# Kernel optimization log

Hardware: AMD Instinct MI355X
Metric: run time of the kernel (lower is better)

The kernel has to match this reference:

```python
import jax, jax.numpy as jnp
import numpy as np

ALPHA = 1.0
LAMBDA_CL = 1.0
EPS = 1e-08


def setup_inputs() -> dict:
    key = jax.random.key(0)
    k1, k2, k3, k4 = jax.random.split(key, 4)
    N, D_IN, D_LAT, K = 16384, 1024, 128, 256
    x = jax.random.normal(k1, (N, D_IN), dtype=jnp.float32)
    h_x = jax.random.normal(k2, (N, D_LAT), dtype=jnp.float32)
    a_x = jax.random.normal(k3, (N, D_IN), dtype=jnp.float32)
    cluster_centers = jax.random.normal(k4, (K, D_LAT), dtype=jnp.float32)
    return {"x": x, "h_x": h_x, "a_x": a_x, "cluster_centers": cluster_centers}


def _pairwise_dist(h, R):
    # Euclidean cdist via ||h||^2 + ||R||^2 - 2 h R^T (avoids [N,K,d] broadcast)
    h2 = jnp.sum(h * h, axis=1, keepdims=True)            # [N,1]
    r2 = jnp.sum(R * R, axis=1)[None, :]                   # [1,K]
    d2 = h2 + r2 - 2.0 * jnp.einsum('nd,kd->nk', h, R)     # [N,K]
    return jnp.sqrt(jnp.maximum(d2, 0.0))


def reference(x, h_x, a_x, cluster_centers):
    # Reconstruction MSE
    loss_reconstr = jnp.mean((x - a_x) ** 2)
    # Alpha-smoothed soft assignments (note +EPS in denominator, as in original)
    dist = _pairwise_dist(h_x, cluster_centers)            # [N,K]
    e = jnp.exp(-ALPHA * dist)                             # [N,K]
    soft_assignments = e / (jnp.sum(e, axis=1, keepdims=True) + EPS)
    # Weighted centers and clustering MSE
    weighted_centers = jnp.einsum('nk,kd->nd', soft_assignments, cluster_centers)
    loss_clustering = jnp.mean((h_x - weighted_centers) ** 2)
    return loss_reconstr + LAMBDA_CL * loss_clustering
```

## Files before the change

kernel.cpp:

```cpp
#include <hip/hip_runtime.h>
#include <math.h>

#define N_ROWS 16384
#define D_INP  1024
#define D_LAT  128
#define KC     256
#define EPS_F  1e-8f

typedef __attribute__((ext_vector_type(8))) short short8v;
typedef _Float16 half8v __attribute__((ext_vector_type(8)));
typedef __attribute__((ext_vector_type(4))) float floatx4;
typedef __attribute__((ext_vector_type(4))) float f4v;

__device__ __forceinline__ unsigned short f2bf(float f) {
    unsigned u = __float_as_uint(f);
    return (unsigned short)((u + 0x7FFFu + ((u >> 16) & 1u)) >> 16);
}
__device__ __forceinline__ unsigned short f2h(float f) {
    _Float16 h = (_Float16)f;
    unsigned short u;
    __builtin_memcpy(&u, &h, 2);
    return u;
}

__global__ __launch_bounds__(256) void prep_kernel(const float* __restrict__ R,
        unsigned short* __restrict__ Rf16, unsigned short* __restrict__ Rtb,
        float* __restrict__ r2) {
    const int t = threadIdx.x;
    const int kc = blockIdx.x * 2 + (t >> 7);
    const int d = t & 127;
    const float v = R[kc * D_LAT + d];
    Rf16[kc * D_LAT + d] = f2h(v);
    Rtb[d * KC + kc] = f2bf(v);
    float sq = v * v;
    for (int off = 32; off > 0; off >>= 1) sq += __shfl_down(sq, off);
    __shared__ float s4[4];
    if ((t & 63) == 0) s4[t >> 6] = sq;
    __syncthreads();
    if (t == 0)   r2[kc] = s4[0] + s4[1];
    if (t == 128) r2[kc] = s4[2] + s4[3];
}

__global__ __launch_bounds__(512) void fused_kernel(
        const float* __restrict__ x, const float* __restrict__ a,
        const float* __restrict__ h,
        const unsigned short* __restrict__ Rf16,
        const unsigned short* __restrict__ Rtb,
        const float* __restrict__ r2w,
        float* __restrict__ pr, float* __restrict__ pc) {
    __shared__ float sh32[16 * 132];
    __shared__ unsigned short sh16[16 * 136];
    __shared__ unsigned short eL[16 * 264];
    __shared__ float sumsL[16][16];
    __shared__ float h2L[16];
    __shared__ float invL[16];
    __shared__ float swL[8];

    const int bid = blockIdx.x;
    const int tid = threadIdx.x;
    const int wv = tid >> 6, lane = tid & 63;

    if (bid & 1) {
        const int rid = bid >> 1;
        const int gid = rid * 512 + tid;
        const f4v* x4 = (const f4v*)x;
        const f4v* a4 = (const f4v*)a;
        float a0 = 0.f, a1 = 0.f, a2 = 0.f, a3 = 0.f;
#pragma unroll
        for (int it = 0; it < 8; ++it) {
            const int i = gid + it * (512 * 1024);
            const f4v xv = __builtin_nontemporal_load(x4 + i);
            const f4v av = __builtin_nontemporal_load(a4 + i);
            const float d0 = xv.x - av.x, d1 = xv.y - av.y;
            const float d2 = xv.z - av.z, d3 = xv.w - av.w;
            a0 = fmaf(d0, d0, a0);
            a1 = fmaf(d1, d1, a1);
            a2 = fmaf(d2, d2, a2);
            a3 = fmaf(d3, d3, a3);
        }
        float acc = (a0 + a1) + (a2 + a3);
        for (int off = 32; off > 0; off >>= 1) acc += __shfl_down(acc, off);
        if (lane == 0) swL[wv] = acc;
        __syncthreads();
        if (tid == 0) {
            float t = 0.f;
#pragma unroll
            for (int w = 0; w < 8; ++w) t += swL[w];
            pr[rid] = t;
        }
        return;
    }

    const int cid = bid >> 1;
    const int rbase = cid * 16;
    const int g = lane >> 4, c = lane & 15;

    {
        const int r = tid >> 5, c4 = tid & 31;
        const f4v v = __builtin_nontemporal_load(
            (const f4v*)(h + (size_t)(rbase + r) * D_LAT + c4 * 4));
        *(f4v*)&sh32[r * 132 + c4 * 4] = v;
        sh16[r * 136 + c4 * 4 + 0] = f2h(v.x);
        sh16[r * 136 + c4 * 4 + 1] = f2h(v.y);
        sh16[r * 136 + c4 * 4 + 2] = f2h(v.z);
        sh16[r * 136 + c4 * 4 + 3] = f2h(v.w);
        float s = v.x * v.x + v.y * v.y + v.z * v.z + v.w * v.w;
        s += __shfl_xor(s, 1);
        s += __shfl_xor(s, 2);
        s += __shfl_xor(s, 4);
        s += __shfl_xor(s, 8);
        s += __shfl_xor(s, 16);
        if ((tid & 31) == 0) h2L[r] = s;
    }
    __syncthreads();

    half8v afr[4];
#pragma unroll
    for (int ks = 0; ks < 4; ++ks)
        afr[ks] = *(const half8v*)&sh16[c * 136 + ks * 32 + g * 8];
    float h2a[4];
#pragma unroll
    for (int i = 0; i < 4; ++i) h2a[i] = h2L[4 * g + i];

#pragma unroll
    for (int tt = 0; tt < 2; ++tt) {
        const int tile = wv * 2 + tt;
        const int kc = tile * 16 + c;
        floatx4 acc = {0.f, 0.f, 0.f, 0.f};
#pragma unroll
        for (int ks = 0; ks < 4; ++ks) {
            const half8v b = *(const half8v*)(Rf16 + (size_t)kc * D_LAT + ks * 32 + g * 8);
            acc = __builtin_amdgcn_mfma_f32_16x16x32_f16(afr[ks], b, acc, 0, 0, 0);
        }
        const float r2v = r2w[kc];
#pragma unroll
        for (int i = 0; i < 4; ++i) {
            const float d2 = h2a[i] + r2v - 2.0f * acc[i];
            const float e = __expf(-sqrtf(fmaxf(d2, 0.f)));
            eL[(4 * g + i) * 264 + kc] = f2bf(e);
            float v = e;
            v += __shfl_xor(v, 1);
            v += __shfl_xor(v, 2);
            v += __shfl_xor(v, 4);
            v += __shfl_xor(v, 8);
            if (c == 0) sumsL[4 * g + i][tile] = v;
        }
    }
    __syncthreads();
    if (tid < 16) {
        float t = 0.f;
#pragma unroll
        for (int j = 0; j < 16; ++j) t += sumsL[tid][j];
        invL[tid] = 1.0f / (t + EPS_F);
    }
    __syncthreads();

    const int dcol = wv * 16 + c;
    float inva[4];
#pragma unroll
    for (int i = 0; i < 4; ++i) inva[i] = invL[4 * g + i];
    floatx4 acc = {0.f, 0.f, 0.f, 0.f};
#pragma unroll
    for (int ks = 0; ks < 8; ++ks) {
        const short8v ae = *(const short8v*)&eL[c * 264 + ks * 32 + g * 8];
        const short8v b = *(const short8v*)(Rtb + (size_t)dcol * KC + ks * 32 + g * 8);
        acc = __builtin_amdgcn_mfma_f32_16x16x32_bf16(ae, b, acc, 0, 0, 0);
    }
    float lp = 0.f;
#pragma unroll
    for (int i = 0; i < 4; ++i) {
        const float wc = acc[i] * inva[i];
        const float hv = sh32[(4 * g + i) * 132 + dcol];
        const float df = hv - wc;
        lp = fmaf(df, df, lp);
    }
    for (int off = 32; off > 0; off >>= 1) lp += __shfl_down(lp, off);
    if (lane == 0) swL[wv] = lp;
    __syncthreads();
    if (tid == 0) {
        float t = 0.f;
#pragma unroll
        for (int w = 0; w < 8; ++w) t += swL[w];
        pc[cid] = t;
    }
}

__global__ __launch_bounds__(256) void finalize_kernel(const float* __restrict__ pr,
                                                       const float* __restrict__ pc,
                                                       float* __restrict__ out) {
    const int tid = threadIdx.x;
    float a = 0.f, b = 0.f;
    for (int i = tid; i < 1024; i += 256) a += pr[i];
    for (int i = tid; i < 1024; i += 256) b += pc[i];
    float v = a * (1.0f / ((float)N_ROWS * (float)D_INP)) +
              b * (1.0f / ((float)N_ROWS * (float)D_LAT));
    for (int off = 32; off > 0; off >>= 1) v += __shfl_down(v, off);
    __shared__ float sw[4];
    if ((tid & 63) == 0) sw[tid >> 6] = v;
    __syncthreads();
    if (tid == 0) out[0] = sw[0] + sw[1] + sw[2] + sw[3];
}

extern "C" void kernel_launch(void* const* d_in, const int* in_sizes, int n_in,
                              void* d_out, int out_size, void* d_ws, size_t ws_size,
                              hipStream_t stream) {
    const float* x = (const float*)d_in[0];
    const float* h = (const float*)d_in[1];
    const float* a = (const float*)d_in[2];
    const float* R = (const float*)d_in[3];
    float* out = (float*)d_out;
    char* wsb = (char*)d_ws;
    float* pr = (float*)(wsb + 0);
    float* pc = (float*)(wsb + 8192);
    float* r2 = (float*)(wsb + 12288);
    unsigned short* Rf16 = (unsigned short*)(wsb + 16384);
    unsigned short* Rtb  = (unsigned short*)(wsb + 16384 + 65536);

    prep_kernel<<<128, 256, 0, stream>>>(R, Rf16, Rtb, r2);
    fused_kernel<<<2048, 512, 0, stream>>>(x, a, h, Rf16, Rtb, r2, pr, pc);
    finalize_kernel<<<1, 256, 0, stream>>>(pr, pc, out);
}
```

Baseline: 48.40 us.

## Process 64 rows per clustering block and rebalance block mix to 1:4

Each clustering block now handles 64 rows instead of 16. It loads the center fragments (Rf16 and a transposed fp16 copy) into registers once and reuses them across four row tiles, which cuts redundant global and L2 reads of the centers. The grid changes from alternating 1:1 to one clustering block per four reconstruction blocks (1280 total), and the reconstruction loads are batched before the arithmetic to raise memory-level parallelism. The second GEMM switches from bf16 to fp16, and the fp32 copy of h is dropped, so the residual now uses the fp16-rounded h. That costs some precision in exchange for less shared memory, which is now larger per block and may reduce occupancy.

```diff
diff --git a/kernel.cpp b/kernel.cpp
--- a/kernel.cpp
+++ b/kernel.cpp
@@ -7,31 +7,31 @@
 #define KC     256
 #define EPS_F  1e-8f
 
-typedef __attribute__((ext_vector_type(8))) short short8v;
 typedef _Float16 half8v __attribute__((ext_vector_type(8)));
 typedef __attribute__((ext_vector_type(4))) float floatx4;
 typedef __attribute__((ext_vector_type(4))) float f4v;
 
-__device__ __forceinline__ unsigned short f2bf(float f) {
-    unsigned u = __float_as_uint(f);
-    return (unsigned short)((u + 0x7FFFu + ((u >> 16) & 1u)) >> 16);
-}
 __device__ __forceinline__ unsigned short f2h(float f) {
     _Float16 h = (_Float16)f;
     unsigned short u;
     __builtin_memcpy(&u, &h, 2);
     return u;
 }
+__device__ __forceinline__ float h2f(unsigned short u) {
+    _Float16 h;
+    __builtin_memcpy(&h, &u, 2);
+    return (float)h;
+}
 
 __global__ __launch_bounds__(256) void prep_kernel(const float* __restrict__ R,
-        unsigned short* __restrict__ Rf16, unsigned short* __restrict__ Rtb,
+        unsigned short* __restrict__ Rf16, unsigned short* __restrict__ Rt16,
         float* __restrict__ r2) {
     const int t = threadIdx.x;
     const int kc = blockIdx.x * 2 + (t >> 7);
     const int d = t & 127;
     const float v = R[kc * D_LAT + d];
     Rf16[kc * D_LAT + d] = f2h(v);
-    Rtb[d * KC + kc] = f2bf(v);
+    Rt16[d * KC + kc] = f2h(v);
     float sq = v * v;
     for (int off = 32; off > 0; off >>= 1) sq += __shfl_down(sq, off);
     __shared__ float s4[4];
@@ -45,34 +45,37 @@
         const float* __restrict__ x, const float* __restrict__ a,
         const float* __restrict__ h,
         const unsigned short* __restrict__ Rf16,
-        const unsigned short* __restrict__ Rtb,
+        const unsigned short* __restrict__ Rt16,
         const float* __restrict__ r2w,
         float* __restrict__ pr, float* __restrict__ pc) {
-    __shared__ float sh32[16 * 132];
-    __shared__ unsigned short sh16[16 * 136];
-    __shared__ unsigned short eL[16 * 264];
-    __shared__ float sumsL[16][16];
-    __shared__ float h2L[16];
-    __shared__ float invL[16];
+    __shared__ unsigned short sh16[64 * 136];
+    __shared__ unsigned short eL[64 * 264];
+    __shared__ float sumsL[64][16];
+    __shared__ float h2L[64];
+    __shared__ float invL[64];
     __shared__ float swL[8];
 
     const int bid = blockIdx.x;
     const int tid = threadIdx.x;
     const int wv = tid >> 6, lane = tid & 63;
 
-    if (bid & 1) {
-        const int rid = bid >> 1;
+    if (bid % 5 != 0) {
+        const int rid = bid - 1 - bid / 5;
         const int gid = rid * 512 + tid;
         const f4v* x4 = (const f4v*)x;
         const f4v* a4 = (const f4v*)a;
-        float a0 = 0.f, a1 = 0.f, a2 = 0.f, a3 = 0.f;
+        f4v xv[8], av[8];
 #pragma unroll
         for (int it = 0; it < 8; ++it) {
             const int i = gid + it * (512 * 1024);
-            const f4v xv = __builtin_nontemporal_load(x4 + i);
-            const f4v av = __builtin_nontemporal_load(a4 + i);
-            const float d0 = xv.x - av.x, d1 = xv.y - av.y;
-            const float d2 = xv.z - av.z, d3 = xv.w - av.w;
+            xv[it] = __builtin_nontemporal_load(x4 + i);
+            av[it] = __builtin_nontemporal_load(a4 + i);
+        }
+        float a0 = 0.f, a1 = 0.f, a2 = 0.f, a3 = 0.f;
+#pragma unroll
+        for (int it = 0; it < 8; ++it) {
+            const float d0 = xv[it].x - av[it].x, d1 = xv[it].y - av[it].y;
+            const float d2 = xv[it].z - av[it].z, d3 = xv[it].w - av[it].w;
             a0 = fmaf(d0, d0, a0);
             a1 = fmaf(d1, d1, a1);
             a2 = fmaf(d2, d2, a2);
@@ -91,63 +94,77 @@
         return;
     }
 
-    const int cid = bid >> 1;
-    const int rbase = cid * 16;
+    const int cid = bid / 5;
+    const int rbase = cid * 64;
     const int g = lane >> 4, c = lane & 15;
 
     {
-        const int r = tid >> 5, c4 = tid & 31;
-        const f4v v = __builtin_nontemporal_load(
-            (const f4v*)(h + (size_t)(rbase + r) * D_LAT + c4 * 4));
-        *(f4v*)&sh32[r * 132 + c4 * 4] = v;
-        sh16[r * 136 + c4 * 4 + 0] = f2h(v.x);
-        sh16[r * 136 + c4 * 4 + 1] = f2h(v.y);
-        sh16[r * 136 + c4 * 4 + 2] = f2h(v.z);
-        sh16[r * 136 + c4 * 4 + 3] = f2h(v.w);
-        float s = v.x * v.x + v.y * v.y + v.z * v.z + v.w * v.w;
+        const int r = tid >> 3, c8 = tid & 7;
+        const float* hrow = h + (size_t)(rbase + r) * D_LAT;
+        float s = 0.f;
+#pragma unroll
+        for (int q = 0; q < 4; ++q) {
+            const int c4 = c8 + q * 8;
+            const f4v v = __builtin_nontemporal_load((const f4v*)(hrow + c4 * 4));
+            sh16[r * 136 + c4 * 4 + 0] = f2h(v.x);
+            sh16[r * 136 + c4 * 4 + 1] = f2h(v.y);
+            sh16[r * 136 + c4 * 4 + 2] = f2h(v.z);
+            sh16[r * 136 + c4 * 4 + 3] = f2h(v.w);
+            s = fmaf(v.x, v.x, s);
+            s = fmaf(v.y, v.y, s);
+            s = fmaf(v.z, v.z, s);
+            s = fmaf(v.w, v.w, s);
+        }
         s += __shfl_xor(s, 1);
         s += __shfl_xor(s, 2);
         s += __shfl_xor(s, 4);
-        s += __shfl_xor(s, 8);
-        s += __shfl_xor(s, 16);
-        if ((tid & 31) == 0) h2L[r] = s;
-    }
-    __syncthreads();
-
-    half8v afr[4];
-#pragma unroll
-    for (int ks = 0; ks < 4; ++ks)
-        afr[ks] = *(const half8v*)&sh16[c * 136 + ks * 32 + g * 8];
-    float h2a[4];
-#pragma unroll
-    for (int i = 0; i < 4; ++i) h2a[i] = h2L[4 * g + i];
-
-#pragma unroll
-    for (int tt = 0; tt < 2; ++tt) {
-        const int tile = wv * 2 + tt;
-        const int kc = tile * 16 + c;
-        floatx4 acc = {0.f, 0.f, 0.f, 0.f};
-#pragma unroll
-        for (int ks = 0; ks < 4; ++ks) {
-            const half8v b = *(const half8v*)(Rf16 + (size_t)kc * D_LAT + ks * 32 + g * 8);
-            acc = __builtin_amdgcn_mfma_f32_16x16x32_f16(afr[ks], b, acc, 0, 0, 0);
-        }
-        const float r2v = r2w[kc];
-#pragma unroll
-        for (int i = 0; i < 4; ++i) {
-            const float d2 = h2a[i] + r2v - 2.0f * acc[i];
-            const float e = __expf(-sqrtf(fmaxf(d2, 0.f)));
-            eL[(4 * g + i) * 264 + kc] = f2bf(e);
-            float v = e;
-            v += __shfl_xor(v, 1);
-            v += __shfl_xor(v, 2);
-            v += __shfl_xor(v, 4);
-            v += __shfl_xor(v, 8);
-            if (c == 0) sumsL[4 * g + i][tile] = v;
-        }
-    }
-    __syncthreads();
-    if (tid < 16) {
+        if ((tid & 7) == 0) h2L[r] = s;
+    }
+    __syncthreads();
+
+    {
+        half8v bA[2][4];
+#pragma unroll
+        for (int tt = 0; tt < 2; ++tt) {
+            const int kc = (wv * 2 + tt) * 16 + c;
+#pragma unroll
+            for (int ks = 0; ks < 4; ++ks)
+                bA[tt][ks] = *(const half8v*)(Rf16 + (size_t)kc * D_LAT + ks * 32 + g * 8);
+        }
+        const float r2v[2] = {r2w[wv * 32 + c], r2w[wv * 32 + 16 + c]};
+#pragma unroll
+        for (int rt = 0; rt < 4; ++rt) {
+            half8v aH[4];
+#pragma unroll
+            for (int ks = 0; ks < 4; ++ks)
+                aH[ks] = *(const half8v*)&sh16[(rt * 16 + c) * 136 + ks * 32 + g * 8];
+            float h2a[4];
+#pragma unroll
+            for (int i = 0; i < 4; ++i) h2a[i] = h2L[rt * 16 + 4 * g + i];
+#pragma unroll
+            for (int tt = 0; tt < 2; ++tt) {
+                floatx4 acc = {0.f, 0.f, 0.f, 0.f};
+#pragma unroll
+                for (int ks = 0; ks < 4; ++ks)
+                    acc = __builtin_amdgcn_mfma_f32_16x16x32_f16(aH[ks], bA[tt][ks], acc, 0, 0, 0);
+                const int kc = (wv * 2 + tt) * 16 + c;
+#pragma unroll
+                for (int i = 0; i < 4; ++i) {
+                    const float d2 = h2a[i] + r2v[tt] - 2.0f * acc[i];
+                    const float e = __expf(-sqrtf(fmaxf(d2, 0.f)));
+                    eL[(rt * 16 + 4 * g + i) * 264 + kc] = f2h(e);
+                    float v = e;
+                    v += __shfl_xor(v, 1);
+                    v += __shfl_xor(v, 2);
+                    v += __shfl_xor(v, 4);
+                    v += __shfl_xor(v, 8);
+                    if (c == 0) sumsL[rt * 16 + 4 * g + i][wv * 2 + tt] = v;
+                }
+            }
+        }
+    }
+    __syncthreads();
+    if (tid < 64) {
         float t = 0.f;
 #pragma unroll
         for (int j = 0; j < 16; ++j) t += sumsL[tid][j];
@@ -155,27 +172,33 @@
     }
     __syncthreads();
 
-    const int dcol = wv * 16 + c;
-    float inva[4];
-#pragma unroll
-    for (int i = 0; i < 4; ++i) inva[i] = invL[4 * g + i];
-    floatx4 acc = {0.f, 0.f, 0.f, 0.f};
-#pragma unroll
-    for (int ks = 0; ks < 8; ++ks) {
-        const short8v ae = *(const short8v*)&eL[c * 264 + ks * 32 + g * 8];
-        const short8v b = *(const short8v*)(Rtb + (size_t)dcol * KC + ks * 32 + g * 8);
-        acc = __builtin_amdgcn_mfma_f32_16x16x32_bf16(ae, b, acc, 0, 0, 0);
-    }
-    float lp = 0.f;
-#pragma unroll
-    for (int i = 0; i < 4; ++i) {
-        const float wc = acc[i] * inva[i];
-        const float hv = sh32[(4 * g + i) * 132 + dcol];
-        const float df = hv - wc;
-        lp = fmaf(df, df, lp);
-    }
-    for (int off = 32; off > 0; off >>= 1) lp += __shfl_down(lp, off);
-    if (lane == 0) swL[wv] = lp;
+    {
+        const int dcol = wv * 16 + c;
+        half8v bB[8];
+#pragma unroll
+        for (int ks = 0; ks < 8; ++ks)
+            bB[ks] = *(const half8v*)(Rt16 + (size_t)dcol * KC + ks * 32 + g * 8);
+        float lp = 0.f;
+#pragma unroll
+        for (int rt = 0; rt < 4; ++rt) {
+            floatx4 acc = {0.f, 0.f, 0.f, 0.f};
+#pragma unroll
+            for (int ks = 0; ks < 8; ++ks) {
+                const half8v ae = *(const half8v*)&eL[(rt * 16 + c) * 264 + ks * 32 + g * 8];
+                acc = __builtin_amdgcn_mfma_f32_16x16x32_f16(ae, bB[ks], acc, 0, 0, 0);
+            }
+#pragma unroll
+            for (int i = 0; i < 4; ++i) {
+                const int row = rt * 16 + 4 * g + i;
+                const float wc = acc[i] * invL[row];
+                const float hv = h2f(sh16[row * 136 + dcol]);
+                const float df = hv - wc;
+                lp = fmaf(df, df, lp);
+            }
+        }
+        for (int off = 32; off > 0; off >>= 1) lp += __shfl_down(lp, off);
+        if (lane == 0) swL[wv] = lp;
+    }
     __syncthreads();
     if (tid == 0) {
         float t = 0.f;
@@ -191,7 +214,7 @@
     const int tid = threadIdx.x;
     float a = 0.f, b = 0.f;
     for (int i = tid; i < 1024; i += 256) a += pr[i];
-    for (int i = tid; i < 1024; i += 256) b += pc[i];
+    if (tid < 256) b = pc[tid];
     float v = a * (1.0f / ((float)N_ROWS * (float)D_INP)) +
               b * (1.0f / ((float)N_ROWS * (float)D_LAT));
     for (int off = 32; off > 0; off >>= 1) v += __shfl_down(v, off);
@@ -214,9 +237,9 @@
     float* pc = (float*)(wsb + 8192);
     float* r2 = (float*)(wsb + 12288);
     unsigned short* Rf16 = (unsigned short*)(wsb + 16384);
-    unsigned short* Rtb  = (unsigned short*)(wsb + 16384 + 65536);
-
-    prep_kernel<<<128, 256, 0, stream>>>(R, Rf16, Rtb, r2);
-    fused_kernel<<<2048, 512, 0, stream>>>(x, a, h, Rf16, Rtb, r2, pr, pc);
+    unsigned short* Rt16 = (unsigned short*)(wsb + 16384 + 65536);
+
+    prep_kernel<<<128, 256, 0, stream>>>(R, Rf16, Rt16, r2);
+    fused_kernel<<<1280, 512, 0, stream>>>(x, a, h, Rf16, Rt16, r2, pr, pc);
     finalize_kernel<<<1, 256, 0, stream>>>(pr, pc, out);
 }
```

Result: faster. 44.61 us (median of 2 runs) (-7.8%).
